# Kernel optimization log

Hardware: AMD Instinct MI355X
Metric: run time of the kernel (lower is better)

The kernel has to match this reference:

```python
import jax, jax.numpy as jnp
import numpy as np

KH, KW = 3, 3
STRIDE = (1, 1)
PAD = 1


def _patches(x):
    # x: (B, C, H, W) -> (B, C, KH, KW, OH, OW)
    B, C, H, W = x.shape
    p = jax.lax.conv_general_dilated_patches(
        x, filter_shape=(KH, KW), window_strides=STRIDE,
        padding=[(PAD, PAD), (PAD, PAD)],
        dimension_numbers=('NCHW', 'OIHW', 'NCHW'))
    OH, OW = p.shape[2], p.shape[3]
    # feature dim of patches is ordered (C, KH, KW) — channel-major
    return p.reshape(B, C, KH, KW, OH, OW)


def setup_inputs() -> dict:
    key = jax.random.key(0)
    k1, k2 = jax.random.split(key, 2)
    B, C, H, W, O = 8, 32, 64, 64, 32
    OH = (H - KH + 2 * PAD) // STRIDE[0] + 1
    OW = (W - KW + 2 * PAD) // STRIDE[1] + 1
    x = jax.random.normal(k1, (B, C, H, W), dtype=jnp.float32)
    # xavier_uniform on the 6D weight (torch fan-in/out convention):
    recf = O * C * KH * KW
    fan_in, fan_out = OW * recf, OH * recf
    limit = float(np.sqrt(6.0 / (fan_in + fan_out)))
    weights = jax.random.uniform(k2, (OH, OW, O, C, KH, KW),
                                 minval=-limit, maxval=limit,
                                 dtype=jnp.float32)
    bias = jnp.zeros((O,), dtype=jnp.float32)
    return {"x": x, "weights": weights, "bias": bias}


def reference(x, weights, bias):
    # locally connected 2D conv: unique weight per output location.
    p = _patches(x)  # (B, C, KH, KW, OH, OW)
    # Faithful to the torch einsum 'bchw,ocwh->bo': the weight's kernel
    # spatial dims (kH,kW) are labeled (w,h), i.e. spatially transposed
    # relative to the patch.
    out = jnp.einsum('bchwij,ijocwh->boij', p, weights)
    return out + bias[None, :, None, None]
```

## Files before the change

### kernel.cpp

```cpp
#include <hip/hip_runtime.h>
#include <hip/hip_bf16.h>


#define NB 8
#define NC 32
#define NO 32
#define NH 64
#define NW 64
#define KK 288
#define LOCS 2
#define XCOLS 4
#define NROWS (NB * NC * 3)
#define XNAT_SZ (NROWS * XCOLS)
#define NSLOT (LOCS * 9 * 32)

typedef __attribute__((ext_vector_type(8))) short s16x8;
typedef __attribute__((ext_vector_type(4))) float f32x4;

union Frag { unsigned short s[8]; uint4 q; s16x8 v; };

__device__ __forceinline__ unsigned short f2bf(float f) {
  __hip_bfloat16 h = __float2bfloat16(f);
  return *reinterpret_cast<unsigned short*>(&h);
}

__global__ __launch_bounds__(256, 4) void lc2d_kernel(
    const float* __restrict__ x, const float* __restrict__ w,
    const float* __restrict__ bias, float* __restrict__ out) {
  const int bid = blockIdx.x;
  const int g = (bid & 7) * 256 + (bid >> 3);
  const int loc0 = g * LOCS;
  const int i = loc0 >> 6;
  const int j0 = loc0 & 63;
  const int t = threadIdx.x;
  const int lane = t & 63;
  const int wv = t >> 6;
  const int m16 = lane & 15;
  const int kg = lane >> 4;
  const int l = wv >> 1;
  const int ot = wv & 1;

  __shared__ float xnat[XNAT_SZ];
  __shared__ uint4 xtb[NSLOT];
  __shared__ float obuf[LOCS][NB][NO];

  float sv[12];
#pragma unroll
  for (int it = 0; it < 12; ++it) {
    int e = t + it * 256;
    int row = e >> 2;
    int cc = e & 3;
    int bc = row / 3;
    int yy = row - bc * 3;
    int y = i + yy - 1;
    int xc = j0 + cc - 1;
    float v = 0.f;
    if ((unsigned)y < 64u && (unsigned)xc < 64u)
      v = x[(bc * NH + y) * NW + xc];
    sv[it] = v;
  }

  float4 wf[18];
  {
    const float* wp =
        w + ((size_t)(loc0 + l) * NO + ot * 16 + m16) * KK + kg * 8;
#pragma unroll
    for (int ks = 0; ks < 9; ++ks) {
      wf[2 * ks]     = *(const float4*)(wp + ks * 32);
      wf[2 * ks + 1] = *(const float4*)(wp + ks * 32 + 4);
    }
  }

#pragma unroll
  for (int it = 0; it < 12; ++it) xnat[t + it * 256] = sv[it];
  asm volatile("s_waitcnt lgkmcnt(0)\n\ts_barrier" ::: "memory");

  for (int sid = t; sid < NSLOT; sid += 256) {
    int l2 = sid / 288;
    int r = sid - l2 * 288;
    int ks = r >> 5;
    int idx = r & 31;
    int bkg = idx >> 3;
    int bm = idx & 7;
    Frag f;
#pragma unroll
    for (int e = 0; e < 8; ++e) {
      int k = ks * 32 + bkg * 8 + e;
      int c = k / 9;
      int rem = k - c * 9;
      int a = rem / 3;
      int bb = rem - a * 3;
      f.s[e] = f2bf(xnat[((bm * NC + c) * 3 + bb) * XCOLS + l2 + a]);
    }
    xtb[sid] = f.q;
  }
  asm volatile("s_waitcnt lgkmcnt(0)\n\ts_barrier" ::: "memory");

  uint4 afr[9];
#pragma unroll
  for (int ks = 0; ks < 9; ++ks)
    afr[ks] = xtb[(l * 9 + ks) * 32 + kg * 8 + (m16 & 7)];

  f32x4 acc = {0.f, 0.f, 0.f, 0.f};
#pragma unroll
  for (int ks = 0; ks < 9; ++ks) {
    float4 lo = wf[2 * ks], hi = wf[2 * ks + 1];
    Frag fb;
    fb.s[0] = f2bf(lo.x); fb.s[1] = f2bf(lo.y);
    fb.s[2] = f2bf(lo.z); fb.s[3] = f2bf(lo.w);
    fb.s[4] = f2bf(hi.x); fb.s[5] = f2bf(hi.y);
    fb.s[6] = f2bf(hi.z); fb.s[7] = f2bf(hi.w);
    Frag fa; fa.q = afr[ks];
    acc = __builtin_amdgcn_mfma_f32_16x16x32_bf16(fa.v, fb.v, acc, 0, 0, 0);
  }

  if (kg < 2) {
#pragma unroll
    for (int r = 0; r < 4; ++r)
      obuf[l][kg * 4 + r][ot * 16 + m16] = acc[r];
  }
  asm volatile("s_waitcnt lgkmcnt(0)\n\ts_barrier" ::: "memory");

  {
    const int b_ = t >> 5;
    const int o_ = t & 31;
    const float bia = bias[o_];
    float2 r2;
    r2.x = obuf[0][b_][o_] + bia;
    r2.y = obuf[1][b_][o_] + bia;
    *reinterpret_cast<float2*>(
        &out[((size_t)(b_ * NO + o_) * NH + i) * NW + j0]) = r2;
  }
}

extern "C" void kernel_launch(void* const* d_in, const int* in_sizes, int n_in,
                              void* d_out, int out_size, void* d_ws, size_t ws_size,
                              hipStream_t stream) {
  const float* x    = (const float*)d_in[0];
  const float* w    = (const float*)d_in[1];
  const float* bias = (const float*)d_in[2];
  float* out = (float*)d_out;
  lc2d_kernel<<<dim3(NH * NW / LOCS), dim3(256), 0, stream>>>(x, w, bias, out);
}
```

Measured before the change: 33.76 us.

## Process four locations per block and build A fragments directly from shared memory

Each block now handles four output locations with 512 threads instead of two with 256, so neighbouring columns share a wider 6-column input halo in shared memory. The separate transposed bf16 staging buffer and its extra barrier are removed; each wave gathers and converts its A fragments straight from the natural-layout tile, using a padded per-batch stride to spread LDS banks. Output stores widen to float4. This cuts redundant input loads and one sync per location pair, but grid size halves and each lane does more scattered LDS reads and conversions.

```diff
diff --git a/kernel.cpp b/kernel.cpp
--- a/kernel.cpp
+++ b/kernel.cpp
@@ -8,11 +8,10 @@
 #define NH 64
 #define NW 64
 #define KK 288
-#define LOCS 2
-#define XCOLS 4
-#define NROWS (NB * NC * 3)
-#define XNAT_SZ (NROWS * XCOLS)
-#define NSLOT (LOCS * 9 * 32)
+#define LOCS 4
+#define XCOLS 6
+#define BSTRIDE 578
+#define XNAT_SZ (NB * BSTRIDE)
 
 typedef __attribute__((ext_vector_type(8))) short s16x8;
 typedef __attribute__((ext_vector_type(4))) float f32x4;
@@ -24,11 +23,11 @@
   return *reinterpret_cast<unsigned short*>(&h);
 }
 
-__global__ __launch_bounds__(256, 4) void lc2d_kernel(
+__global__ __launch_bounds__(512) void lc2d_kernel(
     const float* __restrict__ x, const float* __restrict__ w,
     const float* __restrict__ bias, float* __restrict__ out) {
   const int bid = blockIdx.x;
-  const int g = (bid & 7) * 256 + (bid >> 3);
+  const int g = (bid & 7) * 128 + (bid >> 3);
   const int loc0 = g * LOCS;
   const int i = loc0 >> 6;
   const int j0 = loc0 & 63;
@@ -39,26 +38,29 @@
   const int kg = lane >> 4;
   const int l = wv >> 1;
   const int ot = wv & 1;
+  const int bm = m16 & 7;
 
   __shared__ float xnat[XNAT_SZ];
-  __shared__ uint4 xtb[NSLOT];
   __shared__ float obuf[LOCS][NB][NO];
 
-  float sv[12];
+  float sv[9];
 #pragma unroll
-  for (int it = 0; it < 12; ++it) {
-    int e = t + it * 256;
-    int row = e >> 2;
-    int cc = e & 3;
-    int bc = row / 3;
-    int yy = row - bc * 3;
+  for (int it = 0; it < 9; ++it) {
+    int e = t + it * 512;
+    int b_ = e / 576;
+    int r = e - b_ * 576;
+    int row = r / XCOLS;
+    int cc = r - row * XCOLS;
+    int c = row / 3;
+    int yy = row - c * 3;
     int y = i + yy - 1;
     int xc = j0 + cc - 1;
     float v = 0.f;
     if ((unsigned)y < 64u && (unsigned)xc < 64u)
-      v = x[(bc * NH + y) * NW + xc];
+      v = x[((b_ * NC + c) * NH + y) * NW + xc];
     sv[it] = v;
   }
+  asm volatile("" ::: "memory");
 
   float4 wf[18];
   {
@@ -72,34 +74,29 @@
   }
 
 #pragma unroll
-  for (int it = 0; it < 12; ++it) xnat[t + it * 256] = sv[it];
-  asm volatile("s_waitcnt lgkmcnt(0)\n\ts_barrier" ::: "memory");
-
-  for (int sid = t; sid < NSLOT; sid += 256) {
-    int l2 = sid / 288;
-    int r = sid - l2 * 288;
-    int ks = r >> 5;
-    int idx = r & 31;
-    int bkg = idx >> 3;
-    int bm = idx & 7;
-    Frag f;
-#pragma unroll
-    for (int e = 0; e < 8; ++e) {
-      int k = ks * 32 + bkg * 8 + e;
-      int c = k / 9;
-      int rem = k - c * 9;
-      int a = rem / 3;
-      int bb = rem - a * 3;
-      f.s[e] = f2bf(xnat[((bm * NC + c) * 3 + bb) * XCOLS + l2 + a]);
-    }
-    xtb[sid] = f.q;
+  for (int it = 0; it < 9; ++it) {
+    int e = t + it * 512;
+    int b_ = e / 576;
+    int r = e - b_ * 576;
+    xnat[b_ * BSTRIDE + r] = sv[it];
   }
   asm volatile("s_waitcnt lgkmcnt(0)\n\ts_barrier" ::: "memory");
 
   uint4 afr[9];
 #pragma unroll
-  for (int ks = 0; ks < 9; ++ks)
-    afr[ks] = xtb[(l * 9 + ks) * 32 + kg * 8 + (m16 & 7)];
+  for (int ks = 0; ks < 9; ++ks) {
+    Frag f;
+#pragma unroll
+    for (int e = 0; e < 8; ++e) {
+      int k = ks * 32 + kg * 8 + e;
+      int c = k / 9;
+      int rem = k - c * 9;
+      int a = rem / 3;
+      int bb = rem - a * 3;
+      f.s[e] = f2bf(xnat[bm * BSTRIDE + (c * 3 + bb) * XCOLS + l + a]);
+    }
+    afr[ks] = f.q;
+  }
 
   f32x4 acc = {0.f, 0.f, 0.f, 0.f};
 #pragma unroll
@@ -121,15 +118,17 @@
   }
   asm volatile("s_waitcnt lgkmcnt(0)\n\ts_barrier" ::: "memory");
 
-  {
+  if (t < 256) {
     const int b_ = t >> 5;
     const int o_ = t & 31;
     const float bia = bias[o_];
-    float2 r2;
-    r2.x = obuf[0][b_][o_] + bia;
-    r2.y = obuf[1][b_][o_] + bia;
-    *reinterpret_cast<float2*>(
-        &out[((size_t)(b_ * NO + o_) * NH + i) * NW + j0]) = r2;
+    float4 r4;
+    r4.x = obuf[0][b_][o_] + bia;
+    r4.y = obuf[1][b_][o_] + bia;
+    r4.z = obuf[2][b_][o_] + bia;
+    r4.w = obuf[3][b_][o_] + bia;
+    *reinterpret_cast<float4*>(
+        &out[((size_t)(b_ * NO + o_) * NH + i) * NW + j0]) = r4;
   }
 }
 
@@ -140,5 +139,5 @@
   const float* w    = (const float*)d_in[1];
   const float* bias = (const float*)d_in[2];
   float* out = (float*)d_out;
-  lc2d_kernel<<<dim3(NH * NW / LOCS), dim3(256), 0, stream>>>(x, w, bias, out);
+  lc2d_kernel<<<dim3(NH * NW / LOCS), dim3(512), 0, stream>>>(x, w, bias, out);
 }
```

Measured after the change: 37.06 us. 1.1x slower.
